# Optimization experiments

Measured on AMD Instinct MI355X. Metric: run time of the kernel, lower is better.

The kernel has to match this reference:

```python
import jax, jax.numpy as jnp
import numpy as np

N_EMBD = 1024
N_HEAD = 16
B, T = 4, 2048
EPS = 1e-5


def setup_inputs() -> dict:
    key = jax.random.key(0)
    ks = jax.random.split(key, 12)
    s = 0.02
    d, dff = N_EMBD, 4 * N_EMBD
    return {
        "x": jax.random.normal(ks[0], (B, T, d), dtype=jnp.float32),
        "ln1_w": jnp.ones((d,), jnp.float32),
        "ln1_b": jnp.zeros((d,), jnp.float32),
        "ln2_w": jnp.ones((d,), jnp.float32),
        "ln2_b": jnp.zeros((d,), jnp.float32),
        "w_attn": jax.random.normal(ks[1], (d, 3 * d), jnp.float32) * s,
        "b_attn": jnp.zeros((3 * d,), jnp.float32),
        "w_proj": jax.random.normal(ks[2], (d, d), jnp.float32) * s,
        "b_proj": jnp.zeros((d,), jnp.float32),
        "w_fc": jax.random.normal(ks[3], (d, dff), jnp.float32) * s,
        "b_fc": jnp.zeros((dff,), jnp.float32),
        "w_fc2": jax.random.normal(ks[4], (dff, d), jnp.float32) * s,
        "b_fc2": jnp.zeros((d,), jnp.float32),
    }


def _layernorm(x, w, b):
    mu = jnp.mean(x, axis=-1, keepdims=True)
    var = jnp.mean(jnp.square(x - mu), axis=-1, keepdims=True)
    return (x - mu) * jax.lax.rsqrt(var + EPS) * w + b


def reference(x, ln1_w, ln1_b, ln2_w, ln2_b, w_attn, b_attn, w_proj, b_proj,
              w_fc, b_fc, w_fc2, b_fc2):
    Bx, Tx, C = x.shape
    hd = C // N_HEAD
    # --- attention branch ---
    h = _layernorm(x, ln1_w, ln1_b)
    qkv = h @ w_attn + b_attn  # [B,T,3C]
    q, k, v = jnp.split(qkv, 3, axis=-1)
    q = q.reshape(Bx, Tx, N_HEAD, hd).transpose(0, 2, 1, 3)  # [B,H,T,hd]
    k = k.reshape(Bx, Tx, N_HEAD, hd).transpose(0, 2, 1, 3)
    v = v.reshape(Bx, Tx, N_HEAD, hd).transpose(0, 2, 1, 3)
    att = jnp.einsum("bhqd,bhkd->bhqk", q, k) * (1.0 / np.sqrt(hd))
    causal = jnp.tril(jnp.ones((Tx, Tx), dtype=bool))
    att = jnp.where(causal[None, None], att, -jnp.inf)
    att = jax.nn.softmax(att, axis=-1)
    y = jnp.einsum("bhqk,bhkd->bhqd", att, v)
    y = y.transpose(0, 2, 1, 3).reshape(Bx, Tx, C)
    x = x + (y @ w_proj + b_proj)
    # --- mlp branch ---
    h2 = _layernorm(x, ln2_w, ln2_b)
    m = jax.nn.gelu(h2 @ w_fc + b_fc, approximate=False)
    x = x + (m @ w_fc2 + b_fc2)
    return x
```

## Files before the change

kernel.cpp:

```cpp
#include <hip/hip_runtime.h>
#include <hip/hip_bf16.h>
#include <math.h>

typedef __bf16 bf16;
typedef __bf16 bf16x4 __attribute__((ext_vector_type(4)));
typedef __bf16 bf16x8 __attribute__((ext_vector_type(8)));
typedef float f32x4 __attribute__((ext_vector_type(4)));
typedef unsigned int u32;
typedef unsigned int u32x4 __attribute__((ext_vector_type(4)));

__device__ __forceinline__ void gload_lds16(const bf16* g, bf16* l) {
  __builtin_amdgcn_global_load_lds(
      (const __attribute__((address_space(1))) void*)g,
      (__attribute__((address_space(3))) void*)l, 16, 0, 0);
}

__device__ __forceinline__ u32 pk2(float a, float b) {
  union { bf16 h; unsigned short u; } x, y;
  x.h = (bf16)a; y.h = (bf16)b;
  return (u32)x.u | ((u32)y.u << 16);
}

#define MF(a, b, c) __builtin_amdgcn_mfma_f32_16x16x32_bf16((a), (b), (c), 0, 0, 0)
#define VM2_BAR()  asm volatile("s_waitcnt vmcnt(2)\ns_barrier" ::: "memory")
#define VM0_BAR()  asm volatile("s_waitcnt vmcnt(0)\ns_barrier" ::: "memory")

template <int EPI>
__global__ __launch_bounds__(512, 4)
void gemmk(const bf16* __restrict__ A, const bf16* __restrict__ BT,
           const float* __restrict__ bias, const float* __restrict__ res,
           void* __restrict__ Cout, int M, int N, int K)
{
  __shared__ alignas(16) bf16 lsA[2][8192];
  __shared__ alignas(16) bf16 lsB[2][8192];

  int nbn = N >> 7;
  int nwg = (M >> 7) * nbn;
  int bid = blockIdx.x;
  int cpx = nwg >> 3;
  int wg  = (bid & 7) * cpx + (bid >> 3);
  int m0 = (wg / nbn) << 7;
  int n0 = (wg % nbn) << 7;

  int t = threadIdx.x;
  int l = t & 63, w = t >> 6;
  int gm = w >> 2;
  int gn = w & 3;
  int lr = l & 15, lg = l >> 4;

  int nt = K >> 6;

  const bf16* Ag = A  + (size_t)m0 * K;
  const bf16* Bg = BT + (size_t)n0 * K;

  int swz0 = (lg ^ (lr & 7)) << 3;
  int swz1 = swz0 ^ 32;
  int aBase = (gm * 64 + lr) << 6;
  int bBase = (gn * 32 + lr) << 6;

  int srow = t >> 3;
  int g = (t & 7) ^ (srow & 7);
  const bf16* sA0 = Ag + (size_t)srow * K + g * 8;
  const bf16* sA1 = Ag + (size_t)(64 + srow) * K + g * 8;
  const bf16* sB0 = Bg + (size_t)srow * K + g * 8;
  const bf16* sB1 = Bg + (size_t)(64 + srow) * K + g * 8;
  int dstE = t * 8;

  f32x4 acc[4][2];
  f32x4 zero = {0.f, 0.f, 0.f, 0.f};
#pragma unroll
  for (int mi = 0; mi < 4; ++mi)
#pragma unroll
    for (int ni = 0; ni < 2; ++ni) acc[mi][ni] = zero;

  gload_lds16(sA0, &lsA[0][dstE]);
  gload_lds16(sA1, &lsA[0][4096 + dstE]);
  gload_lds16(sB0, &lsB[0][dstE]);
  gload_lds16(sB1, &lsB[0][4096 + dstE]);

  bf16x8 af[4][2], bf[2][2];

  for (int T = 0; T < nt; ++T) {
    int c = T & 1, d = c ^ 1;
    bool st = (T + 1 < nt);
    int k64 = (T + 1) << 6;

    VM2_BAR();
#pragma unroll
    for (int mi = 0; mi < 4; ++mi) {
      af[mi][0] = *(const bf16x8*)(&lsA[c][0] + aBase + mi * 1024 + swz0);
      af[mi][1] = *(const bf16x8*)(&lsA[c][0] + aBase + mi * 1024 + swz1);
    }
    if (st) {
      gload_lds16(sA0 + k64, &lsA[d][dstE]);
      gload_lds16(sA1 + k64, &lsA[d][4096 + dstE]);
    }

    if (st) VM2_BAR(); else VM0_BAR();
#pragma unroll
    for (int ni = 0; ni < 2; ++ni) {
      bf[ni][0] = *(const bf16x8*)(&lsB[c][0] + bBase + ni * 1024 + swz0);
      bf[ni][1] = *(const bf16x8*)(&lsB[c][0] + bBase + ni * 1024 + swz1);
    }
    if (st) {
      gload_lds16(sB0 + k64, &lsB[d][dstE]);
      gload_lds16(sB1 + k64, &lsB[d][4096 + dstE]);
    }
    __builtin_amdgcn_s_setprio(1);
#pragma unroll
    for (int mi = 0; mi < 4; ++mi)
#pragma unroll
      for (int ni = 0; ni < 2; ++ni)
#pragma unroll
        for (int kk = 0; kk < 2; ++kk)
          acc[mi][ni] = MF(af[mi][kk], bf[ni][kk], acc[mi][ni]);
    __builtin_amdgcn_s_setprio(0);
  }

  const float SCLQ = 0.18033688011112042f;
  bf16* Pb = (bf16*)Cout;
#pragma unroll
  for (int mi = 0; mi < 4; ++mi) {
    int row = m0 + gm * 64 + mi * 16 + lg * 4;
#pragma unroll
    for (int ni = 0; ni < 2; ++ni) {
      int col = n0 + gn * 32 + ni * 16 + lr;
      float bv = bias[col];
      f32x4 a = acc[mi][ni];
#pragma unroll
      for (int r = 0; r < 4; ++r) {
        float v = a[r] + bv;
        size_t idx = (size_t)(row + r) * N + col;
        if (EPI == 0)      Pb[idx] = (bf16)v;
        else if (EPI == 1) ((float*)Cout)[idx] = v + res[idx];
        else if (EPI == 2) Pb[idx] = (bf16)(0.5f * v * (1.f + erff(v * 0.70710678118654752f)));
        else if (EPI == 4) Pb[idx] = (bf16)((col < 1024) ? v * SCLQ : v);
      }
    }
  }
}

__global__ __launch_bounds__(256)
void ln_bf16(const float* __restrict__ x, const float* __restrict__ w,
             const float* __restrict__ b, bf16* __restrict__ out)
{
  int row = blockIdx.x;
  int t = threadIdx.x;
  float4 v = ((const float4*)(x + (size_t)row * 1024))[t];
  float s  = v.x + v.y + v.z + v.w;
  float sq = v.x * v.x + v.y * v.y + v.z * v.z + v.w * v.w;
#pragma unroll
  for (int off = 32; off >= 1; off >>= 1) {
    s  += __shfl_xor(s, off);
    sq += __shfl_xor(sq, off);
  }
  __shared__ float ps[4], pq[4];
  if ((t & 63) == 0) { ps[t >> 6] = s; pq[t >> 6] = sq; }
  __syncthreads();
  s  = ps[0] + ps[1] + ps[2] + ps[3];
  sq = pq[0] + pq[1] + pq[2] + pq[3];
  float mu  = s * (1.f / 1024.f);
  float var = sq * (1.f / 1024.f) - mu * mu;
  float rstd = rsqrtf(var + 1e-5f);
  float4 wv = ((const float4*)w)[t];
  float4 bv = ((const float4*)b)[t];
  size_t o0 = (size_t)row * 1024 + t * 4;
  out[o0 + 0] = (bf16)((v.x - mu) * rstd * wv.x + bv.x);
  out[o0 + 1] = (bf16)((v.y - mu) * rstd * wv.y + bv.y);
  out[o0 + 2] = (bf16)((v.z - mu) * rstd * wv.z + bv.z);
  out[o0 + 3] = (bf16)((v.w - mu) * rstd * wv.w + bv.w);
}

__global__ __launch_bounds__(256)
void transpose_cast(const float* __restrict__ W, bf16* __restrict__ WT, int K, int N)
{
  __shared__ float tile[32][33];
  int bk = blockIdx.x * 32, bn = blockIdx.y * 32;
  int tx = threadIdx.x & 31, ty = threadIdx.x >> 5;
#pragma unroll
  for (int i = ty; i < 32; i += 8)
    tile[i][tx] = W[(size_t)(bk + i) * N + bn + tx];
  __syncthreads();
#pragma unroll
  for (int i = ty; i < 32; i += 8)
    WT[(size_t)(bn + i) * K + bk + tx] = (bf16)tile[tx][i];
}

__global__ __launch_bounds__(256)
void vtrans(const bf16* __restrict__ qkv, bf16* __restrict__ vt)
{
  __shared__ alignas(16) bf16 tile[64 * 64];
  int bh = blockIdx.x;
  int b = bh >> 4, h = bh & 15;
  int t0 = blockIdx.y * 64;
  int t = threadIdx.x;
#pragma unroll
  for (int i = 0; i < 2; ++i) {
    int c = i * 256 + t;
    int tt = c >> 3, d8 = c & 7;
    bf16x8 v = *(const bf16x8*)(qkv + (size_t)(b * 2048 + t0 + tt) * 3072 + 2048 + h * 64 + d8 * 8);
    *(bf16x8*)&tile[(tt * 8 + (d8 ^ (tt >> 3))) * 8] = v;
  }
  __syncthreads();
#pragma unroll
  for (int i = 0; i < 2; ++i) {
    int c = i * 256 + t;
    int d = c >> 3, tt8 = c & 7;
    bf16x8 o;
#pragma unroll
    for (int j = 0; j < 8; ++j) {
      int row = tt8 * 8 + j;
      o[j] = tile[(row * 8 + ((d >> 3) ^ (row >> 3))) * 8 + (d & 7)];
    }
    *(bf16x8*)(vt + (size_t)(bh * 64 + d) * 2048 + t0 + tt8 * 8) = o;
  }
}

__global__ __launch_bounds__(512)
void attn_flash(const bf16* __restrict__ qkv, const bf16* __restrict__ vt,
                bf16* __restrict__ y)
{
  __shared__ alignas(16) bf16 lk[2][4096];
  __shared__ alignas(16) bf16 lv[2][4096];

  int bid = blockIdx.x;
  int bh = bid & 63;
  int qb = 15 - (bid >> 6);
  int b = bh >> 4, h = bh & 15;
  int t = threadIdx.x;
  int w = t >> 6, l = t & 63;
  int lr = l & 15, lg = l >> 4;
  int q0 = qb * 128;
  int qw = q0 + w * 16;
  const size_t RS = 3072;

  const bf16* qbase = qkv + (size_t)(b * 2048) * RS + h * 64;
  const bf16* kbase = qkv + (size_t)(b * 2048) * RS + 1024 + h * 64;
  const bf16* vtb   = vt + (size_t)(bh * 64) * 2048;

  bf16x8 qf[2];
#pragma unroll
  for (int kk = 0; kk < 2; ++kk)
    qf[kk] = *(const bf16x8*)(qbase + (size_t)(qw + lr) * RS + kk * 32 + lg * 8);

  int row = t >> 3, c8 = t & 7;
  int sc8 = c8 ^ (row & 7);
  const bf16* pK = kbase + (size_t)row * RS + sc8 * 8;
  const bf16* pV = vtb + (size_t)row * 2048 + sc8 * 8;
  int dst = t * 8;

  f32x4 zero = {0.f, 0.f, 0.f, 0.f};
  f32x4 o[4];
#pragma unroll
  for (int ni = 0; ni < 4; ++ni) o[ni] = zero;
  float lo = 0.f;

  int srcA = lr + ((lg & 1) << 5);
  int srcB = srcA + 16;
  int jhalf = lg >> 1;

  int nkb = 2 * qb + 2;
  gload_lds16(pK, &lk[0][dst]);
  gload_lds16(pV, &lv[0][dst]);

  for (int kb = 0; kb < nkb; ++kb) {
    int cur = kb & 1;
    int k0 = kb * 64;
    VM0_BAR();
    if (kb + 1 < nkb) {
      pK += 64 * RS;
      pV += 64;
      gload_lds16(pK, &lk[cur ^ 1][dst]);
      gload_lds16(pV, &lv[cur ^ 1][dst]);
    }
    if (k0 > qw + 15) continue;

    f32x4 s[4];
#pragma unroll
    for (int j = 0; j < 4; ++j) s[j] = zero;
#pragma unroll
    for (int kk = 0; kk < 2; ++kk)
#pragma unroll
      for (int j = 0; j < 4; ++j) {
        int krow = j * 16 + lr;
        bf16x8 kf = *(const bf16x8*)&lk[cur][krow * 64 + (((4 * kk + lg) ^ (krow & 7)) * 8)];
        s[j] = MF(kf, qf[kk], s[j]);
      }

    bool needmask = (k0 + 63 > qw);
    u32 packL[4], packH[4];
#pragma unroll
    for (int j = 0; j < 4; ++j) {
      int kbase_j = k0 + j * 16 + lg * 4;
      int tq = qw + lr;
      float v0 = s[j][0], v1 = s[j][1], v2 = s[j][2], v3 = s[j][3];
      if (needmask) {
        if (kbase_j + 0 > tq) v0 = -1e30f;
        if (kbase_j + 1 > tq) v1 = -1e30f;
        if (kbase_j + 2 > tq) v2 = -1e30f;
        if (kbase_j + 3 > tq) v3 = -1e30f;
      }
      float p0 = exp2f(v0), p1 = exp2f(v1), p2 = exp2f(v2), p3 = exp2f(v3);
      lo += (p0 + p1) + (p2 + p3);
      packL[j] = pk2(p0, p1);
      packH[j] = pk2(p2, p3);
    }

#pragma unroll
    for (int kf = 0; kf < 2; ++kf) {
      u32 la0 = __shfl(packL[2 * kf], srcA), la1 = __shfl(packL[2 * kf + 1], srcA);
      u32 ha0 = __shfl(packH[2 * kf], srcA), ha1 = __shfl(packH[2 * kf + 1], srcA);
      u32 lb0 = __shfl(packL[2 * kf], srcB), lb1 = __shfl(packL[2 * kf + 1], srcB);
      u32 hb0 = __shfl(packH[2 * kf], srcB), hb1 = __shfl(packH[2 * kf + 1], srcB);
      u32x4 pa32;
      pa32[0] = jhalf ? la1 : la0;
      pa32[1] = jhalf ? ha1 : ha0;
      pa32[2] = jhalf ? lb1 : lb0;
      pa32[3] = jhalf ? hb1 : hb0;
      bf16x8 pa = __builtin_bit_cast(bf16x8, pa32);
#pragma unroll
      for (int ni = 0; ni < 4; ++ni) {
        int d = ni * 16 + lr;
        bf16x8 vf = *(const bf16x8*)&lv[cur][d * 64 + (((4 * kf + lg) ^ (d & 7)) * 8)];
        o[ni] = MF(pa, vf, o[ni]);
      }
    }
  }

  lo += __shfl_xor(lo, 16);
  lo += __shfl_xor(lo, 32);
  float inv[4];
#pragma unroll
  for (int r = 0; r < 4; ++r)
    inv[r] = 1.f / __shfl(lo, (lg << 4) | (lg * 4 + r));
#pragma unroll
  for (int ni = 0; ni < 4; ++ni)
#pragma unroll
    for (int r = 0; r < 4; ++r) {
      int tq = qw + lg * 4 + r;
      y[(size_t)(b * 2048 + tq) * 1024 + h * 64 + ni * 16 + lr] = (bf16)(o[ni][r] * inv[r]);
    }
}

extern "C" void kernel_launch(void* const* d_in, const int* in_sizes, int n_in,
                              void* d_out, int out_size, void* d_ws, size_t ws_size,
                              hipStream_t stream) {
  (void)in_sizes; (void)n_in; (void)out_size; (void)ws_size;
  const float* x      = (const float*)d_in[0];
  const float* ln1w   = (const float*)d_in[1];
  const float* ln1b   = (const float*)d_in[2];
  const float* ln2w   = (const float*)d_in[3];
  const float* ln2b   = (const float*)d_in[4];
  const float* w_attn = (const float*)d_in[5];
  const float* b_attn = (const float*)d_in[6];
  const float* w_proj = (const float*)d_in[7];
  const float* b_proj = (const float*)d_in[8];
  const float* w_fc   = (const float*)d_in[9];
  const float* b_fc   = (const float*)d_in[10];
  const float* w_fc2  = (const float*)d_in[11];
  const float* b_fc2  = (const float*)d_in[12];
  float* out = (float*)d_out;

  char* p = (char*)d_ws;
  bf16*  h     = (bf16*)p;  p += (size_t)8192 * 1024 * 2;
  bf16*  qkv   = (bf16*)p;
  bf16*  mbuf  = (bf16*)p;  p += (size_t)8192 * 3072 * 2;
  bf16*  ybuf  = (bf16*)p;  p += (size_t)8192 * 1024 * 2;
  float* x1    = (float*)p; p += (size_t)8192 * 1024 * 4;
  bf16*  wqkvT = (bf16*)p;  p += (size_t)3072 * 1024 * 2;
  bf16*  wprojT= (bf16*)p;  p += (size_t)1024 * 1024 * 2;
  bf16*  wfcT  = (bf16*)p;  p += (size_t)4096 * 1024 * 2;
  bf16*  wfc2T = (bf16*)p;  p += (size_t)1024 * 4096 * 2;
  bf16*  vt    = (bf16*)x1;

  transpose_cast<<<dim3(1024 / 32, 3072 / 32), 256, 0, stream>>>(w_attn, wqkvT, 1024, 3072);
  transpose_cast<<<dim3(1024 / 32, 1024 / 32), 256, 0, stream>>>(w_proj, wprojT, 1024, 1024);
  transpose_cast<<<dim3(1024 / 32, 4096 / 32), 256, 0, stream>>>(w_fc,   wfcT,  1024, 4096);
  transpose_cast<<<dim3(4096 / 32, 1024 / 32), 256, 0, stream>>>(w_fc2,  wfc2T, 4096, 1024);

  ln_bf16<<<8192, 256, 0, stream>>>(x, ln1w, ln1b, h);
  gemmk<4><<<1536, 512, 0, stream>>>(h, wqkvT, b_attn, nullptr, qkv, 8192, 3072, 1024);
  vtrans<<<dim3(64, 32), 256, 0, stream>>>(qkv, vt);
  attn_flash<<<1024, 512, 0, stream>>>(qkv, vt, ybuf);
  gemmk<1><<<512, 512, 0, stream>>>(ybuf, wprojT, b_proj, x, x1, 8192, 1024, 1024);
  ln_bf16<<<8192, 256, 0, stream>>>(x1, ln2w, ln2b, h);
  gemmk<2><<<2048, 512, 0, stream>>>(h, wfcT, b_fc, nullptr, mbuf, 8192, 4096, 1024);
  gemmk<1><<<512, 512, 0, stream>>>(mbuf, wfc2T, b_fc2, x1, out, 8192, 1024, 4096);
}
```

Measured before the change: 388.4 us.

## Store residual intermediate in bf16 and regroup GEMM tile rasterization

The attention-projection GEMM now writes the residual sum x1 as bf16 instead of fp32. A new bf16-input LayerNorm reads it, and the final GEMM adds the bf16 residual back in fp32. This halves the memory traffic for the intermediate residual but loses precision in the residual stream. The GEMM workgroup mapping also changes to sweep groups of four N-tiles down all M-tiles, to change L2 reuse of the weights versus activations. The vt buffer gets its own workspace region instead of aliasing x1.

```diff
diff --git a/kernel.cpp b/kernel.cpp
--- a/kernel.cpp
+++ b/kernel.cpp
@@ -28,19 +28,22 @@
 template <int EPI>
 __global__ __launch_bounds__(512, 4)
 void gemmk(const bf16* __restrict__ A, const bf16* __restrict__ BT,
-           const float* __restrict__ bias, const float* __restrict__ res,
+           const float* __restrict__ bias, const void* __restrict__ res,
            void* __restrict__ Cout, int M, int N, int K)
 {
   __shared__ alignas(16) bf16 lsA[2][8192];
   __shared__ alignas(16) bf16 lsB[2][8192];
 
   int nbn = N >> 7;
-  int nwg = (M >> 7) * nbn;
+  int nbm = M >> 7;
+  int nwg = nbm * nbn;
   int bid = blockIdx.x;
   int cpx = nwg >> 3;
   int wg  = (bid & 7) * cpx + (bid >> 3);
-  int m0 = (wg / nbn) << 7;
-  int n0 = (wg % nbn) << 7;
+  int sg  = wg / (nbm * 4);
+  int rem = wg - sg * (nbm * 4);
+  int m0 = (rem >> 2) << 7;
+  int n0 = (sg * 4 + (rem & 3)) << 7;
 
   int t = threadIdx.x;
   int l = t & 63, w = t >> 6;
@@ -119,6 +122,8 @@
 
   const float SCLQ = 0.18033688011112042f;
   bf16* Pb = (bf16*)Cout;
+  const float* resf = (const float*)res;
+  const bf16* resh = (const bf16*)res;
 #pragma unroll
   for (int mi = 0; mi < 4; ++mi) {
     int row = m0 + gm * 64 + mi * 16 + lg * 4;
@@ -132,9 +137,10 @@
         float v = a[r] + bv;
         size_t idx = (size_t)(row + r) * N + col;
         if (EPI == 0)      Pb[idx] = (bf16)v;
-        else if (EPI == 1) ((float*)Cout)[idx] = v + res[idx];
         else if (EPI == 2) Pb[idx] = (bf16)(0.5f * v * (1.f + erff(v * 0.70710678118654752f)));
         else if (EPI == 4) Pb[idx] = (bf16)((col < 1024) ? v * SCLQ : v);
+        else if (EPI == 5) Pb[idx] = (bf16)(v + resf[idx]);
+        else if (EPI == 6) ((float*)Cout)[idx] = v + (float)resh[idx];
       }
     }
   }
@@ -169,6 +175,38 @@
   out[o0 + 1] = (bf16)((v.y - mu) * rstd * wv.y + bv.y);
   out[o0 + 2] = (bf16)((v.z - mu) * rstd * wv.z + bv.z);
   out[o0 + 3] = (bf16)((v.w - mu) * rstd * wv.w + bv.w);
+}
+
+__global__ __launch_bounds__(256)
+void lnh_bf16(const bf16* __restrict__ x, const float* __restrict__ w,
+              const float* __restrict__ b, bf16* __restrict__ out)
+{
+  int row = blockIdx.x;
+  int t = threadIdx.x;
+  bf16x4 hv = *(const bf16x4*)(x + (size_t)row * 1024 + t * 4);
+  float v0 = (float)hv[0], v1 = (float)hv[1], v2 = (float)hv[2], v3 = (float)hv[3];
+  float s  = v0 + v1 + v2 + v3;
+  float sq = v0 * v0 + v1 * v1 + v2 * v2 + v3 * v3;
+#pragma unroll
+  for (int off = 32; off >= 1; off >>= 1) {
+    s  += __shfl_xor(s, off);
+    sq += __shfl_xor(sq, off);
+  }
+  __shared__ float ps[4], pq[4];
+  if ((t & 63) == 0) { ps[t >> 6] = s; pq[t >> 6] = sq; }
+  __syncthreads();
+  s  = ps[0] + ps[1] + ps[2] + ps[3];
+  sq = pq[0] + pq[1] + pq[2] + pq[3];
+  float mu  = s * (1.f / 1024.f);
+  float var = sq * (1.f / 1024.f) - mu * mu;
+  float rstd = rsqrtf(var + 1e-5f);
+  float4 wv = ((const float4*)w)[t];
+  float4 bv = ((const float4*)b)[t];
+  size_t o0 = (size_t)row * 1024 + t * 4;
+  out[o0 + 0] = (bf16)((v0 - mu) * rstd * wv.x + bv.x);
+  out[o0 + 1] = (bf16)((v1 - mu) * rstd * wv.y + bv.y);
+  out[o0 + 2] = (bf16)((v2 - mu) * rstd * wv.z + bv.z);
+  out[o0 + 3] = (bf16)((v3 - mu) * rstd * wv.w + bv.w);
 }
 
 __global__ __launch_bounds__(256)
@@ -366,12 +404,12 @@
   bf16*  qkv   = (bf16*)p;
   bf16*  mbuf  = (bf16*)p;  p += (size_t)8192 * 3072 * 2;
   bf16*  ybuf  = (bf16*)p;  p += (size_t)8192 * 1024 * 2;
-  float* x1    = (float*)p; p += (size_t)8192 * 1024 * 4;
+  bf16*  x1h   = (bf16*)p;  p += (size_t)8192 * 1024 * 2;
+  bf16*  vt    = (bf16*)p;  p += (size_t)8192 * 2048 * 2;
   bf16*  wqkvT = (bf16*)p;  p += (size_t)3072 * 1024 * 2;
   bf16*  wprojT= (bf16*)p;  p += (size_t)1024 * 1024 * 2;
   bf16*  wfcT  = (bf16*)p;  p += (size_t)4096 * 1024 * 2;
   bf16*  wfc2T = (bf16*)p;  p += (size_t)1024 * 4096 * 2;
-  bf16*  vt    = (bf16*)x1;
 
   transpose_cast<<<dim3(1024 / 32, 3072 / 32), 256, 0, stream>>>(w_attn, wqkvT, 1024, 3072);
   transpose_cast<<<dim3(1024 / 32, 1024 / 32), 256, 0, stream>>>(w_proj, wprojT, 1024, 1024);
@@ -382,8 +420,8 @@
   gemmk<4><<<1536, 512, 0, stream>>>(h, wqkvT, b_attn, nullptr, qkv, 8192, 3072, 1024);
   vtrans<<<dim3(64, 32), 256, 0, stream>>>(qkv, vt);
   attn_flash<<<1024, 512, 0, stream>>>(qkv, vt, ybuf);
-  gemmk<1><<<512, 512, 0, stream>>>(ybuf, wprojT, b_proj, x, x1, 8192, 1024, 1024);
-  ln_bf16<<<8192, 256, 0, stream>>>(x1, ln2w, ln2b, h);
+  gemmk<5><<<512, 512, 0, stream>>>(ybuf, wprojT, b_proj, x, x1h, 8192, 1024, 1024);
+  lnh_bf16<<<8192, 256, 0, stream>>>(x1h, ln2w, ln2b, h);
   gemmk<2><<<2048, 512, 0, stream>>>(h, wfcT, b_fc, nullptr, mbuf, 8192, 4096, 1024);
-  gemmk<1><<<512, 512, 0, stream>>>(mbuf, wfc2T, b_fc2, x1, out, 8192, 1024, 4096);
-}
+  gemmk<6><<<512, 512, 0, stream>>>(mbuf, wfc2T, b_fc2, x1h, out, 8192, 1024, 4096);
+}
```

After: 372.8 us. 4.0% less time.
